# Kernel optimization log

Measured on AMD Instinct MI355X. Metric: run time of the kernel, lower is better.

Reference implementation:

```python
import jax, jax.numpy as jnp
import numpy as np

B, N, DQ, DK, DV = 8, 2048, 1024, 1024, 1024

def setup_inputs() -> dict:
    key = jax.random.key(0)
    kx, kq, kk, kv = jax.random.split(key, 4)
    x = jax.random.normal(kx, (B, N, DQ), dtype=jnp.float32)
    # nn.Linear(dim_q, dim_k, bias=False) weights: [out, in]
    s = 1.0 / np.sqrt(DQ)
    Wq = jax.random.uniform(kq, (DK, DQ), jnp.float32, -s, s)
    Wk = jax.random.uniform(kk, (DK, DQ), jnp.float32, -s, s)
    Wv = jax.random.uniform(kv, (DV, DQ), jnp.float32, -s, s)
    return {"x": x, "Wq": Wq, "Wk": Wk, "Wv": Wv}

def reference(x, Wq, Wk, Wv):
    batch, n, _ = x.shape
    q = jnp.einsum('bnd,kd->bnk', x, Wq)  # [B,n,DK]
    k = jnp.einsum('bnd,kd->bnk', x, Wk)  # [B,n,DK]
    v = jnp.einsum('bnd,vd->bnv', x, Wv)  # [B,n,DV]
    norm = 1.0 / jnp.sqrt(jnp.asarray(Wq.shape[0], jnp.float32))
    dist = jnp.einsum('bik,bjk->bij', q, k) * norm  # [B,n,n]
    causal = jnp.tril(jnp.ones((n, n), dtype=bool))
    dist = jnp.where(causal[None, :, :], dist, jnp.float32(-1e20))
    dist = jax.nn.softmax(dist, axis=-1)
    att = jnp.einsum('bij,bjv->biv', dist, v)  # [B,n,DV]
    return att
```

## Files before the change

kernel.cpp:

```cpp
#include <hip/hip_runtime.h>
#include <hip/hip_bf16.h>

typedef __attribute__((ext_vector_type(4))) float floatx4;
typedef __bf16 bf16x8 __attribute__((ext_vector_type(8)));
typedef unsigned int u32;
typedef unsigned short u16;

typedef __attribute__((address_space(1))) const u32 g_u32;
typedef __attribute__((address_space(3))) u32 l_u32;

__device__ __forceinline__ u16 f32_to_bf16(float f) {
    union { float f; u32 u; } x{f};
    u32 u = x.u;
    u32 r = (u + 0x7fffu + ((u >> 16) & 1u)) >> 16;
    return (u16)r;
}


__device__ __forceinline__ void stage_half_sw(const u16* gbase, int ld, u16* lds_half, int tid) {
    int lane = tid & 63;
    int rsub = lane >> 3;
    int colsw = ((lane & 7) ^ rsub) << 3;
#pragma unroll
    for (int j = 0; j < 2; ++j) {
        int q = (tid >> 6) * 2 + j;
        int row = q * 8 + rsub;
        const u16* g = gbase + (long)row * ld + colsw;
        u16* l = lds_half + q * 512 + lane * 8;
        __builtin_amdgcn_global_load_lds((g_u32*)g, (l_u32*)l, 16, 0, 0);
    }
}

#define EIGHT_PHASE_LOOP(Ab, Bb, lda, ldb, ITERS, TMAX)                                \
    stage_half_sw(Bb,                  ldb, &Bs[0][0],        tid);                    \
    stage_half_sw(Bb + 128 * (ldb),    ldb, &Bs[0][128 * 64], tid);                    \
    stage_half_sw(Ab,                  lda, &As[0][0],        tid);                    \
    stage_half_sw(Ab + 128 * (lda),    lda, &As[0][128 * 64], tid);                    \
    stage_half_sw(Bb + 64,             ldb, &Bs[1][0],        tid);                    \
    stage_half_sw(Bb + 64 + 128 * (ldb), ldb, &Bs[1][128 * 64], tid);                  \
    asm volatile("s_waitcnt vmcnt(4)" ::: "memory");                                   \
    __builtin_amdgcn_sched_barrier(0);                                                 \
    __builtin_amdgcn_s_barrier();                                                      \
    for (int i = 0; i < (ITERS); ++i) {                                                \
        int t1  = 2 * i + 1;                                                           \
        int tn  = (2 * i + 2 <= (TMAX)) ? 2 * i + 2 : (TMAX);                          \
        int tn1 = (2 * i + 3 <= (TMAX)) ? 2 * i + 3 : (TMAX);                          \
        const u16* gA1 = Ab + t1 * 64;                                                 \
        const u16* gB2 = Bb + tn * 64;                                                 \
        const u16* gA2 = Ab + tn * 64;                                                 \
        const u16* gB3 = Bb + tn1 * 64;                                                \
        bf16x8 bq0[4], bq1[4];                                                         \
        _Pragma("unroll")                                                              \
        for (int half = 0; half < 2; ++half) {                                         \
            _Pragma("unroll")                                                          \
            for (int p = 0; p < 4; ++p) {                                              \
                if (p == 0) {                                                          \
                    _Pragma("unroll")                                                  \
                    for (int ni = 0; ni < 4; ++ni) {                                   \
                        bq0[ni] = *(const bf16x8*)&Bs[half][brow + ni * 1024 + sl0];   \
                        bq1[ni] = *(const bf16x8*)&Bs[half][brow + ni * 1024 + sl1];   \
                    }                                                                  \
                }                                                                      \
                bf16x8 a00 = *(const bf16x8*)&As[half][arow + (2 * p)     * 1024 + sl0]; \
                bf16x8 a01 = *(const bf16x8*)&As[half][arow + (2 * p)     * 1024 + sl1]; \
                bf16x8 a10 = *(const bf16x8*)&As[half][arow + (2 * p + 1) * 1024 + sl0]; \
                bf16x8 a11 = *(const bf16x8*)&As[half][arow + (2 * p + 1) * 1024 + sl1]; \
                int ph = half * 4 + p;                                                 \
                switch (ph) {                                                          \
                    case 0: stage_half_sw(gA1,              lda, &As[1][0],        tid); break; \
                    case 1: stage_half_sw(gA1 + 128 * (lda), lda, &As[1][128 * 64], tid); break; \
                    case 2: stage_half_sw(gB2,              ldb, &Bs[0][0],        tid); break; \
                    case 3: stage_half_sw(gB2 + 128 * (ldb), ldb, &Bs[0][128 * 64], tid); break; \
                    case 4: stage_half_sw(gA2,              lda, &As[0][0],        tid); break; \
                    case 5: stage_half_sw(gA2 + 128 * (lda), lda, &As[0][128 * 64], tid); break; \
                    case 6: stage_half_sw(gB3,              ldb, &Bs[1][0],        tid); break; \
                    case 7: stage_half_sw(gB3 + 128 * (ldb), ldb, &Bs[1][128 * 64], tid); break; \
                }                                                                      \
                __builtin_amdgcn_s_barrier();                                          \
                __builtin_amdgcn_s_setprio(1);                                         \
                int m0 = 2 * p;                                                        \
                _Pragma("unroll")                                                      \
                for (int ni = 0; ni < 4; ++ni) {                                       \
                    acc[m0][ni]     = __builtin_amdgcn_mfma_f32_16x16x32_bf16(a00, bq0[ni], acc[m0][ni],     0, 0, 0); \
                    acc[m0][ni]     = __builtin_amdgcn_mfma_f32_16x16x32_bf16(a01, bq1[ni], acc[m0][ni],     0, 0, 0); \
                    acc[m0 + 1][ni] = __builtin_amdgcn_mfma_f32_16x16x32_bf16(a10, bq0[ni], acc[m0 + 1][ni], 0, 0, 0); \
                    acc[m0 + 1][ni] = __builtin_amdgcn_mfma_f32_16x16x32_bf16(a11, bq1[ni], acc[m0 + 1][ni], 0, 0, 0); \
                }                                                                      \
                __builtin_amdgcn_s_setprio(0);                                         \
                if (p == 3) {                                                          \
                    asm volatile("s_waitcnt vmcnt(4)" ::: "memory");                   \
                    __builtin_amdgcn_sched_barrier(0);                                 \
                }                                                                      \
                __builtin_amdgcn_s_barrier();                                          \
            }                                                                          \
        }                                                                              \
    }                                                                                  \
    asm volatile("s_waitcnt vmcnt(0)" ::: "memory");                                   \
    __builtin_amdgcn_sched_barrier(0);

__global__ __launch_bounds__(512, 2)
void qkv_gemm8(const u16* __restrict__ A, const u16* __restrict__ Bw,
               u16* __restrict__ QKi, u16* __restrict__ Vt)
{
    __shared__ u16 As[2][256 * 64];
    __shared__ u16 Bs[2][256 * 64];

    int bid = blockIdx.x;
    int wg = (bid & 7) * 96 + (bid >> 3);
    int mt = wg / 12, nt = wg - mt * 12;

    int tid = threadIdx.x;
    int lane = tid & 63, wv = tid >> 6;
    int wr = wv >> 2, wc = wv & 3;
    int lrow = lane & 15, quad = lane >> 4;
    int sw = lrow & 7;

    const u16* Ab = A + (long)mt * 256 * 1024;
    const u16* Bb = Bw + (long)nt * 256 * 1024;

    floatx4 acc[8][4] = {};
    const int arow = (wr * 128 + lrow) * 64;
    const int brow = (wc * 64 + lrow) * 64;
    const int sl0 = (quad ^ sw) * 8;
    const int sl1 = ((4 + quad) ^ sw) * 8;

    EIGHT_PHASE_LOOP(Ab, Bb, 1024, 1024, 8, 15)

    if (nt < 8) {
        long crow0 = (long)mt * 256 + wr * 128 + quad * 4;
        int  ccol0 = nt * 256 + wc * 64 + lrow;
#pragma unroll
        for (int mi = 0; mi < 8; ++mi) {
#pragma unroll
            for (int r = 0; r < 4; ++r) {
                long row = crow0 + mi * 16 + r;
#pragma unroll
                for (int ni = 0; ni < 4; ++ni)
                    QKi[row * 2048 + ccol0 + ni * 16] = f32_to_bf16(acc[mi][ni][r]);
            }
        }
    } else {
        int dv0   = (nt - 8) * 256 + wc * 64 + lrow;
        long tok0 = (long)mt * 256 + wr * 128 + quad * 4;
#pragma unroll
        for (int mi = 0; mi < 8; ++mi) {
#pragma unroll
            for (int ni = 0; ni < 4; ++ni) {
                ushort4 o;
                o.x = f32_to_bf16(acc[mi][ni][0]);
                o.y = f32_to_bf16(acc[mi][ni][1]);
                o.z = f32_to_bf16(acc[mi][ni][2]);
                o.w = f32_to_bf16(acc[mi][ni][3]);
                *(ushort4*)(Vt + (long)(dv0 + ni * 16) * 16384 + tok0 + mi * 16) = o;
            }
        }
    }
}

__global__ __launch_bounds__(512, 2)
void s_gemm8(const u16* __restrict__ QKi, u16* __restrict__ P, float* __restrict__ lsum)
{
    __shared__ u16 As[2][256 * 64];
    __shared__ u16 Bs[2][256 * 64];

    int bid = blockIdx.x;
    int b  = bid & 7;
    int ti = bid >> 3;
    int mt = (int)((__builtin_sqrtf(8.0f * ti + 1.0f) - 1.0f) * 0.5f);
    while ((mt + 1) * (mt + 2) / 2 <= ti) ++mt;
    while (mt * (mt + 1) / 2 > ti) --mt;
    int nt = ti - mt * (mt + 1) / 2;

    int tid = threadIdx.x;
    int lane = tid & 63, wv = tid >> 6;
    int wr = wv >> 2, wc = wv & 3;
    int lrow = lane & 15, quad = lane >> 4;
    int sw = lrow & 7;

    const u16* Qb = QKi + (long)b * 2048 * 2048 + (long)mt * 256 * 2048;
    const u16* Kb = QKi + (long)b * 2048 * 2048 + (long)nt * 256 * 2048 + 1024;
    u16* Pb = P + (long)b * 2048 * 2048;
    float* ls = lsum + b * 2048;

    floatx4 acc[8][4] = {};
    const int arow = (wr * 128 + lrow) * 64;
    const int brow = (wc * 64 + lrow) * 64;
    const int sl0 = (quad ^ sw) * 8;
    const int sl1 = ((4 + quad) ^ sw) * 8;

    EIGHT_PHASE_LOOP(Qb, Kb, 2048, 2048, 8, 15)

    int crow0 = mt * 256 + wr * 128 + quad * 4;
    int ccol0 = nt * 256 + wc * 64 + lrow;
#pragma unroll
    for (int mi = 0; mi < 8; ++mi) {
#pragma unroll
        for (int r = 0; r < 4; ++r) {
            int row = crow0 + mi * 16 + r;
            float rs = 0.f;
#pragma unroll
            for (int ni = 0; ni < 4; ++ni) {
                int col = ccol0 + ni * 16;
                float v = acc[mi][ni][r] * 0.03125f;
                float e = (col > row) ? 0.f : __expf(v);
                Pb[(long)row * 2048 + col] = f32_to_bf16(e);
                rs += e;
            }
            rs += __shfl_xor(rs, 1, 16);
            rs += __shfl_xor(rs, 2, 16);
            rs += __shfl_xor(rs, 4, 16);
            rs += __shfl_xor(rs, 8, 16);
            if (lrow == 0) atomicAdd(&ls[row], rs);
        }
    }
}

__global__ __launch_bounds__(512, 2)
void pv_gemm8(const u16* __restrict__ P, const u16* __restrict__ Vt,
              float* __restrict__ O, const float* __restrict__ lsum)
{
    __shared__ u16 As[2][256 * 64];
    __shared__ u16 Bs[2][256 * 64];

    int bid = blockIdx.x;
    int b  = bid & 7;
    int r2 = bid >> 3;
    int mt = r2 >> 2;
    int nt = r2 & 3;

    int tid = threadIdx.x;
    int lane = tid & 63, wv = tid >> 6;
    int wr = wv >> 2, wc = wv & 3;
    int lrow = lane & 15, quad = lane >> 4;
    int sw = lrow & 7;

    const u16* Ab = P  + (long)b * 2048 * 2048 + (long)mt * 256 * 2048;
    const u16* Bb = Vt + (long)nt * 256 * 16384 + b * 2048;
    float* Ob = O + (long)b * 2048 * 1024;
    const float* ls = lsum + b * 2048;

    int iters = (mt + 1) * 2;
    int tmax  = (mt + 1) * 4 - 1;

    floatx4 acc[8][4] = {};
    const int arow = (wr * 128 + lrow) * 64;
    const int brow = (wc * 64 + lrow) * 64;
    const int sl0 = (quad ^ sw) * 8;
    const int sl1 = ((4 + quad) ^ sw) * 8;

    EIGHT_PHASE_LOOP(Ab, Bb, 2048, 16384, iters, tmax)

    int crow0 = mt * 256 + wr * 128 + quad * 4;
    int ccol0 = nt * 256 + wc * 64 + lrow;
#pragma unroll
    for (int mi = 0; mi < 8; ++mi) {
#pragma unroll
        for (int r = 0; r < 4; ++r) {
            int row = crow0 + mi * 16 + r;
            float linv = 1.0f / ls[row];
#pragma unroll
            for (int ni = 0; ni < 4; ++ni)
                Ob[(long)row * 1024 + ccol0 + ni * 16] = acc[mi][ni][r] * linv;
        }
    }
}

__global__ __launch_bounds__(256)
void cvt_all(const float* __restrict__ x, const float* __restrict__ Wq,
             const float* __restrict__ Wk, const float* __restrict__ Wv,
             u16* __restrict__ xb, u16* __restrict__ wb, float* __restrict__ lsum)
{
    int bb = blockIdx.x;
    if (bb < 16384) {
        long idx = ((long)bb * 256 + threadIdx.x) << 2;
        float4 f = *(const float4*)(x + idx);
        ushort4 o;
        o.x = f32_to_bf16(f.x); o.y = f32_to_bf16(f.y);
        o.z = f32_to_bf16(f.z); o.w = f32_to_bf16(f.w);
        *(ushort4*)(xb + idx) = o;
    } else if (bb < 16384 + 3072) {
        int wbk = bb - 16384;
        int which = wbk >> 10;
        const float* src = which == 0 ? Wq : (which == 1 ? Wk : Wv);
        long base = (long)(wbk & 1023) * 1024 + threadIdx.x * 4;
        float4 f = *(const float4*)(src + base);
        ushort4 o;
        o.x = f32_to_bf16(f.x); o.y = f32_to_bf16(f.y);
        o.z = f32_to_bf16(f.z); o.w = f32_to_bf16(f.w);
        *(ushort4*)(wb + (long)which * 1048576 + base) = o;
    } else {
        long idx = ((long)(bb - 16384 - 3072) * 256 + threadIdx.x) << 2;
        *(float4*)(lsum + idx) = float4{0.f, 0.f, 0.f, 0.f};
    }
}

extern "C" void kernel_launch(void* const* d_in, const int* in_sizes, int n_in,
                              void* d_out, int out_size, void* d_ws, size_t ws_size,
                              hipStream_t stream)
{
    const int B = 8, N = 2048, D = 1024;
    const long MT = (long)B * N;
    const long nX = MT * D;
    const long nW = (long)D * D;

    const float* x  = (const float*)d_in[0];
    const float* Wq = (const float*)d_in[1];
    const float* Wk = (const float*)d_in[2];
    const float* Wv = (const float*)d_in[3];
    float* out = (float*)d_out;

    u16* wb   = (u16*)d_ws;
    u16* xb   = wb + 3 * nW;
    u16* QKi  = xb + nX;
    u16* Vt   = QKi + MT * 2048;
    u16* P    = Vt + nX;
    float* lsum = (float*)(P + (long)B * N * N);

    cvt_all<<<16384 + 3072 + 16, 256, 0, stream>>>(x, Wq, Wk, Wv, xb, wb, lsum);

    qkv_gemm8<<<dim3(768, 1, 1), 512, 0, stream>>>(xb, wb, QKi, Vt);

    s_gemm8<<<dim3(288, 1, 1), 512, 0, stream>>>(QKi, P, lsum);

    pv_gemm8<<<dim3(256, 1, 1), 512, 0, stream>>>(P, Vt, out, lsum);
}
```

Baseline: 350.0 us.

## Fuse all stages into one cooperative persistent kernel with per-row flags

```diff
diff --git a/kernel.cpp b/kernel.cpp
--- a/kernel.cpp
+++ b/kernel.cpp
@@ -1,5 +1,8 @@
 #include <hip/hip_runtime.h>
 #include <hip/hip_bf16.h>
+#include <hip/hip_cooperative_groups.h>
+
+namespace cg = cooperative_groups;
 
 typedef __attribute__((ext_vector_type(4))) float floatx4;
 typedef __bf16 bf16x8 __attribute__((ext_vector_type(8)));
@@ -98,18 +101,12 @@
     asm volatile("s_waitcnt vmcnt(0)" ::: "memory");                                   \
     __builtin_amdgcn_sched_barrier(0);
 
-__global__ __launch_bounds__(512, 2)
-void qkv_gemm8(const u16* __restrict__ A, const u16* __restrict__ Bw,
-               u16* __restrict__ QKi, u16* __restrict__ Vt)
-{
-    __shared__ u16 As[2][256 * 64];
-    __shared__ u16 Bs[2][256 * 64];
-
-    int bid = blockIdx.x;
-    int wg = (bid & 7) * 96 + (bid >> 3);
-    int mt = wg / 12, nt = wg - mt * 12;
-
-    int tid = threadIdx.x;
+typedef u16 lds_t[256 * 64];
+
+__device__ __forceinline__ void qkv_unit(int mt, int nt,
+    const u16* __restrict__ A, const u16* __restrict__ Bw,
+    u16* __restrict__ QKi, u16* __restrict__ Vt, lds_t* As, lds_t* Bs, int tid)
+{
     int lane = tid & 63, wv = tid >> 6;
     int wr = wv >> 2, wc = wv & 3;
     int lrow = lane & 15, quad = lane >> 4;
@@ -157,21 +154,10 @@
     }
 }
 
-__global__ __launch_bounds__(512, 2)
-void s_gemm8(const u16* __restrict__ QKi, u16* __restrict__ P, float* __restrict__ lsum)
-{
-    __shared__ u16 As[2][256 * 64];
-    __shared__ u16 Bs[2][256 * 64];
-
-    int bid = blockIdx.x;
-    int b  = bid & 7;
-    int ti = bid >> 3;
-    int mt = (int)((__builtin_sqrtf(8.0f * ti + 1.0f) - 1.0f) * 0.5f);
-    while ((mt + 1) * (mt + 2) / 2 <= ti) ++mt;
-    while (mt * (mt + 1) / 2 > ti) --mt;
-    int nt = ti - mt * (mt + 1) / 2;
-
-    int tid = threadIdx.x;
+__device__ __forceinline__ void s_unit(int b, int mt, int nt,
+    const u16* __restrict__ QKi, u16* __restrict__ P, float* __restrict__ lsum,
+    int* __restrict__ srow, lds_t* As, lds_t* Bs, int tid)
+{
     int lane = tid & 63, wv = tid >> 6;
     int wr = wv >> 2, wc = wv & 3;
     int lrow = lane & 15, quad = lane >> 4;
@@ -213,22 +199,25 @@
             if (lrow == 0) atomicAdd(&ls[row], rs);
         }
     }
-}
-
-__global__ __launch_bounds__(512, 2)
-void pv_gemm8(const u16* __restrict__ P, const u16* __restrict__ Vt,
-              float* __restrict__ O, const float* __restrict__ lsum)
-{
-    __shared__ u16 As[2][256 * 64];
-    __shared__ u16 Bs[2][256 * 64];
-
-    int bid = blockIdx.x;
-    int b  = bid & 7;
-    int r2 = bid >> 3;
-    int mt = r2 >> 2;
-    int nt = r2 & 3;
-
-    int tid = threadIdx.x;
+    __syncthreads();
+    if (tid == 0) {
+        __builtin_amdgcn_fence(__ATOMIC_RELEASE, "agent");
+        __hip_atomic_fetch_add(&srow[b * 8 + mt], 1, __ATOMIC_RELAXED, __HIP_MEMORY_SCOPE_AGENT);
+    }
+}
+
+__device__ __forceinline__ void pv_unit(int b, int mt, int nt,
+    const u16* __restrict__ P, const u16* __restrict__ Vt, float* __restrict__ O,
+    const float* __restrict__ lsum, int* __restrict__ srow, lds_t* As, lds_t* Bs, int tid)
+{
+    if (tid == 0) {
+        while (__hip_atomic_load(&srow[b * 8 + mt], __ATOMIC_RELAXED, __HIP_MEMORY_SCOPE_AGENT) < mt + 1)
+            __builtin_amdgcn_s_sleep(8);
+    }
+    __syncthreads();
+    __builtin_amdgcn_fence(__ATOMIC_ACQUIRE, "agent");
+    __builtin_amdgcn_sched_barrier(0);
+
     int lane = tid & 63, wv = tid >> 6;
     int wr = wv >> 2, wc = wv & 3;
     int lrow = lane & 15, quad = lane >> 4;
@@ -265,33 +254,93 @@
     }
 }
 
-__global__ __launch_bounds__(256)
-void cvt_all(const float* __restrict__ x, const float* __restrict__ Wq,
-             const float* __restrict__ Wk, const float* __restrict__ Wv,
-             u16* __restrict__ xb, u16* __restrict__ wb, float* __restrict__ lsum)
-{
-    int bb = blockIdx.x;
-    if (bb < 16384) {
-        long idx = ((long)bb * 256 + threadIdx.x) << 2;
-        float4 f = *(const float4*)(x + idx);
-        ushort4 o;
-        o.x = f32_to_bf16(f.x); o.y = f32_to_bf16(f.y);
-        o.z = f32_to_bf16(f.z); o.w = f32_to_bf16(f.w);
-        *(ushort4*)(xb + idx) = o;
-    } else if (bb < 16384 + 3072) {
-        int wbk = bb - 16384;
-        int which = wbk >> 10;
-        const float* src = which == 0 ? Wq : (which == 1 ? Wk : Wv);
-        long base = (long)(wbk & 1023) * 1024 + threadIdx.x * 4;
-        float4 f = *(const float4*)(src + base);
-        ushort4 o;
-        o.x = f32_to_bf16(f.x); o.y = f32_to_bf16(f.y);
-        o.z = f32_to_bf16(f.z); o.w = f32_to_bf16(f.w);
-        *(ushort4*)(wb + (long)which * 1048576 + base) = o;
+__device__ __forceinline__ void s_decode(int idx, int& b, int& mt, int& nt) {
+    int start = 0;
+    for (int m = 6; m >= 0; --m) {
+        int cnt = 8 * (m + 1);
+        if (idx < start + cnt) {
+            int l = idx - start;
+            b = l / (m + 1);
+            nt = l - b * (m + 1);
+            mt = m;
+            return;
+        }
+        start += cnt;
+    }
+    b = 0; mt = 0; nt = 0;
+}
+
+__global__ void __launch_bounds__(512, 2) mega(
+    const float* __restrict__ x, const float* __restrict__ Wq,
+    const float* __restrict__ Wk, const float* __restrict__ Wv,
+    u16* __restrict__ xb, u16* __restrict__ wb, u16* __restrict__ QKi,
+    u16* __restrict__ Vt, u16* __restrict__ P, float* __restrict__ lsum,
+    int* __restrict__ srow, float* __restrict__ out)
+{
+    __shared__ u16 As[2][256 * 64];
+    __shared__ u16 Bs[2][256 * 64];
+    cg::grid_group grid = cg::this_grid();
+    int bid = blockIdx.x, tid = threadIdx.x;
+
+    {
+        long base = (long)bid * 512 + tid;
+        const float4* x4 = (const float4*)x;
+        ushort4* xb4 = (ushort4*)xb;
+#pragma unroll 4
+        for (int it = 0; it < 32; ++it) {
+            long u = base + (long)it * 131072;
+            float4 f = x4[u];
+            ushort4 o;
+            o.x = f32_to_bf16(f.x); o.y = f32_to_bf16(f.y);
+            o.z = f32_to_bf16(f.z); o.w = f32_to_bf16(f.w);
+            xb4[u] = o;
+        }
+#pragma unroll
+        for (int it = 0; it < 6; ++it) {
+            long u = base + (long)it * 131072;
+            int which = (int)(u >> 18);
+            long off = u & 262143;
+            const float4* src = (const float4*)(which == 0 ? Wq : (which == 1 ? Wk : Wv));
+            float4 f = src[off];
+            ushort4 o;
+            o.x = f32_to_bf16(f.x); o.y = f32_to_bf16(f.y);
+            o.z = f32_to_bf16(f.z); o.w = f32_to_bf16(f.w);
+            ((ushort4*)wb)[u] = o;
+        }
+        if (bid < 8) ((float4*)lsum)[bid * 512 + tid] = float4{0.f, 0.f, 0.f, 0.f};
+        if (bid == 8 && tid < 64) srow[tid] = 0;
+    }
+    grid.sync();
+
+    for (int k = 0; k < 3; ++k) {
+        int u = k * 256 + bid;
+        int wg = (u & 7) * 96 + (u >> 3);
+        int mt = wg / 12, nt = wg - mt * 12;
+        qkv_unit(mt, nt, xb, wb, QKi, Vt, As, Bs, tid);
+    }
+    grid.sync();
+
+    int sb[2], smt[2], snt[2], ns;
+    int pb, pmt, pnt;
+    if (bid < 64) {
+        ns = 1; sb[0] = bid >> 3; smt[0] = 7; snt[0] = bid & 7;
+        int j = bid & 7; pb = bid >> 3;
+        if (j < 4) { pmt = 7; pnt = j; } else { pmt = 6; pnt = j - 4; }
+    } else if (bid < 96) {
+        int i = bid - 64; ns = 2;
+        s_decode(160 + i, sb[0], smt[0], snt[0]);
+        s_decode(192 + i, sb[1], smt[1], snt[1]);
+        pb = i >> 2; pmt = 0; pnt = i & 3;
     } else {
-        long idx = ((long)(bb - 16384 - 3072) * 256 + threadIdx.x) << 2;
-        *(float4*)(lsum + idx) = float4{0.f, 0.f, 0.f, 0.f};
-    }
+        int c = bid - 96; ns = 1;
+        s_decode(c, sb[0], smt[0], snt[0]);
+        pmt = 1 + c / 32; int sub = c & 31; pb = sub >> 2; pnt = sub & 3;
+    }
+
+    for (int k = 0; k < ns; ++k)
+        s_unit(sb[k], smt[k], snt[k], QKi, P, lsum, srow, As, Bs, tid);
+
+    pv_unit(pb, pmt, pnt, P, Vt, out, lsum, srow, As, Bs, tid);
 }
 
 extern "C" void kernel_launch(void* const* d_in, const int* in_sizes, int n_in,
@@ -315,12 +364,12 @@
     u16* Vt   = QKi + MT * 2048;
     u16* P    = Vt + nX;
     float* lsum = (float*)(P + (long)B * N * N);
-
-    cvt_all<<<16384 + 3072 + 16, 256, 0, stream>>>(x, Wq, Wk, Wv, xb, wb, lsum);
-
-    qkv_gemm8<<<dim3(768, 1, 1), 512, 0, stream>>>(xb, wb, QKi, Vt);
-
-    s_gemm8<<<dim3(288, 1, 1), 512, 0, stream>>>(QKi, P, lsum);
-
-    pv_gemm8<<<dim3(256, 1, 1), 512, 0, stream>>>(P, Vt, out, lsum);
-}
+    int* srow = (int*)(lsum + 16384);
+
+    void* kargs[] = {
+        (void*)&x, (void*)&Wq, (void*)&Wk, (void*)&Wv,
+        (void*)&xb, (void*)&wb, (void*)&QKi, (void*)&Vt,
+        (void*)&P, (void*)&lsum, (void*)&srow, (void*)&out
+    };
+    hipLaunchCooperativeKernel((void*)mega, dim3(256), dim3(512), kargs, 0, stream);
+}
```

New measurement: 446.9 us. 27.7% more time.
